# Kernel optimization log

Measured on AMD Instinct MI355X. Metric: run time of the kernel, lower is better.

Reference implementation:

```python
import jax, jax.numpy as jnp
import numpy as np

SEQ_LEN = 8192
D_MODEL = 1024
D_K = 128
D_V = 128


def setup_inputs() -> dict:
    key = jax.random.key(0)
    kx, kq, kk, kv = jax.random.split(key, 4)
    # xavier-uniform scale for (out, in) linear weights
    def xavier(k, out_f, in_f):
        lim = np.sqrt(6.0 / (in_f + out_f))
        return jax.random.uniform(k, (out_f, in_f), jnp.float32, -lim, lim)
    return {
        "X": jax.random.normal(kx, (SEQ_LEN, D_MODEL), jnp.float32),
        "Wq": xavier(kq, D_K, D_MODEL),
        "Wk": xavier(kk, D_K, D_MODEL),
        "Wv": xavier(kv, D_V, D_MODEL),
    }


def reference(X, Wq, Wk, Wv):
    # X: (S, d_model); W*: (d_k, d_model) torch Linear weights (y = x @ W.T)
    S = X.shape[0]
    Q = X @ Wq.T                      # (S, d_k)
    K = X @ Wk.T                      # (S, d_k)
    V = X @ Wv.T                      # (S, d_v)
    scale = jnp.sqrt(jnp.asarray(D_K, X.dtype))
    scores = (Q @ K.T) / scale        # (S, S)
    causal = jnp.tril(jnp.ones((S, S), bool))
    scores = jnp.where(causal, scores, -jnp.inf)
    weights = jax.nn.softmax(scores, axis=1)
    # dropout p=0.0 -> identity
    Z = weights @ V                   # (S, d_v)
    return Z
```

## Files before the change

### kernel.cpp

```cpp
#include <hip/hip_runtime.h>
#include <hip/hip_bf16.h>

#define S_LEN 8192
#define DM    1024
#define DK    128
#define KSTR  136
#define VSTR  72
#define SLOTD 2112
#define NCMAX 16

typedef __attribute__((ext_vector_type(8))) short bf16x8;
typedef __attribute__((ext_vector_type(8))) _Float16 f16x8;
typedef __attribute__((ext_vector_type(4))) float f32x4;
typedef __attribute__((ext_vector_type(16))) float f32x16;

__device__ __forceinline__ f32x4 mfma16f(f16x8 a, f16x8 b, f32x4 c) {
    return __builtin_amdgcn_mfma_f32_16x16x32_f16(a, b, c, 0, 0, 0);
}
__device__ __forceinline__ f32x16 mfma32(bf16x8 a, bf16x8 b, f32x16 c) {
    return __builtin_amdgcn_mfma_f32_32x32x16_bf16(a, b, c, 0, 0, 0);
}

__device__ __forceinline__ ushort f2bf(float f) {
    unsigned u = __builtin_bit_cast(unsigned, f);
    u += 0x7FFFu + ((u >> 16) & 1u);
    return (ushort)(u >> 16);
}

__device__ __forceinline__ ushort f2h(float f) {
    return __builtin_bit_cast(ushort, (_Float16)f);
}

__device__ __forceinline__ uint cvt_pk_bf16(float a, float b) {
    uint r;
    asm("v_cvt_pk_bf16_f32 %0, %1, %2" : "=v"(r) : "v"(a), "v"(b));
    return r;
}

__global__ __launch_bounds__(256, 1)
void convert_w_kernel(const float* __restrict__ Wq,
                      const float* __restrict__ Wk,
                      const float* __restrict__ Wv,
                      _Float16* __restrict__ Wh) {
    const int NW4 = DK * DM / 4;
    const int i = blockIdx.x * 256 + threadIdx.x;
    const int which = i / NW4;
    const int off = i - which * NW4;
    const float4 v = ((const float4*)(which == 0 ? Wq : (which == 1 ? Wk : Wv)))[off];
    union { _Float16 h[4]; uint2 u; } p;
    p.h[0] = (_Float16)v.x; p.h[1] = (_Float16)v.y;
    p.h[2] = (_Float16)v.z; p.h[3] = (_Float16)v.w;
    *(uint2*)(Wh + (size_t)which * (DK * DM) + (size_t)off * 4) = p.u;
}

__global__ __launch_bounds__(256)
void proj_gemm_kernel(const float* __restrict__ X,
                      const _Float16* __restrict__ Wh,
                      ushort* __restrict__ Qb,
                      ushort* __restrict__ Kb,
                      ushort* __restrict__ Vtb) {
    __shared__ _Float16 Ash[2][16 * 32];
    __shared__ _Float16 Bsh[2][384 * 32];

    const int tid  = threadIdx.x;
    const int lane = tid & 63;
    const int quad = lane >> 4;
    const int l15  = lane & 15;
    const int wv   = tid >> 6;
    const int m0   = blockIdx.x * 16;
    const int arow = tid >> 3, ac4 = tid & 7;

    f32x4 acc[3][2];
#pragma unroll
    for (int nb = 0; nb < 3; ++nb)
#pragma unroll
        for (int ni = 0; ni < 2; ++ni) acc[nb][ni] = (f32x4){0.f, 0.f, 0.f, 0.f};

#define STAGE_B(KK, BUF)                                                       \
    {                                                                          \
        _Pragma("unroll")                                                      \
        for (int s_ = tid; s_ < 1536; s_ += 256) {                             \
            const int row_ = s_ >> 2, sg_ = s_ & 3;                            \
            __builtin_amdgcn_global_load_lds(                                  \
                (const __attribute__((address_space(1))) void*)(Wh + (size_t)row_ * DM + (KK) + sg_ * 8), \
                (__attribute__((address_space(3))) void*)(Bsh[BUF] + s_ * 8), 16, 0, 0); \
        }                                                                      \
    }
#define LOAD_A(DST, KK)                                                        \
    if (tid < 128) (DST) = *(const float4*)(X + (size_t)(m0 + arow) * DM + (KK) + ac4 * 4);
#define WRITE_A(SRC, BUF)                                                      \
    if (tid < 128) {                                                           \
        union { _Float16 h[4]; uint2 u; } pa_;                                 \
        pa_.h[0] = (_Float16)(SRC).x; pa_.h[1] = (_Float16)(SRC).y;            \
        pa_.h[2] = (_Float16)(SRC).z; pa_.h[3] = (_Float16)(SRC).w;            \
        *(uint2*)(Ash[BUF] + arow * 32 + ac4 * 4) = pa_.u;                     \
    }
#define COMPUTE(BUF)                                                           \
    {                                                                          \
        const f16x8 af_ = *(const f16x8*)(Ash[BUF] + l15 * 32 + quad * 8);     \
        _Pragma("unroll")                                                      \
        for (int nb_ = 0; nb_ < 3; ++nb_)                                      \
            _Pragma("unroll")                                                  \
            for (int ni_ = 0; ni_ < 2; ++ni_) {                                \
                const f16x8 bf_ = *(const f16x8*)(Bsh[BUF] + (nb_ * 128 + wv * 32 + ni_ * 16 + l15) * 32 + quad * 8); \
                acc[nb_][ni_] = mfma16f(af_, bf_, acc[nb_][ni_]);              \
            }                                                                  \
    }

    float4 ra, rb;
    LOAD_A(ra, 0)
    LOAD_A(rb, 32)
    STAGE_B(0, 0)
    WRITE_A(ra, 0)
    __syncthreads();

    for (int kk = 0; kk < DM; kk += 64) {
        if (kk + 32 < DM) STAGE_B(kk + 32, 1)
        if (kk + 64 < DM) LOAD_A(ra, kk + 64)
        COMPUTE(0)
        if (kk + 32 < DM) WRITE_A(rb, 1)
        __syncthreads();
        if (kk + 32 < DM) {
            if (kk + 64 < DM) STAGE_B(kk + 64, 0)
            if (kk + 96 < DM) LOAD_A(rb, kk + 96)
            COMPUTE(1)
            if (kk + 64 < DM) WRITE_A(ra, 0)
            __syncthreads();
        }
    }
#undef STAGE_B
#undef LOAD_A
#undef WRITE_A
#undef COMPUTE

    const float scq = 0.088388347648318447f * 1.4426950408889634f;
#pragma unroll
    for (int ni = 0; ni < 2; ++ni) {
        const int n = wv * 32 + ni * 16 + l15;
#pragma unroll
        for (int r = 0; r < 4; ++r)
            Qb[(size_t)(m0 + quad * 4 + r) * DK + n] = f2bf(acc[0][ni][r] * scq);
#pragma unroll
        for (int r = 0; r < 4; ++r)
            Kb[(size_t)(m0 + quad * 4 + r) * DK + n] = f2bf(acc[1][ni][r]);
        union { ushort h[4]; uint2 u; } p;
#pragma unroll
        for (int r = 0; r < 4; ++r) p.h[r] = f2bf(acc[2][ni][r]);
        *(uint2*)(Vtb + (size_t)n * S_LEN + m0 + quad * 4) = p.u;
    }
}

__global__ __launch_bounds__(256, 2)
void flash_partial_kernel(const ushort* __restrict__ Qg,
                          const ushort* __restrict__ Kg,
                          const ushort* __restrict__ Vtg,
                          float* __restrict__ Part) {
    __shared__ __align__(16) ushort Ks [2][64 * KSTR];
    __shared__ __align__(16) ushort Vts[2][128 * VSTR];

    int rem = 543 - (int)blockIdx.x;
    int qb = 0;
    for (;;) {
        const int nc = (2 * qb + 9) >> 3;
        if (rem < nc) break;
        rem -= nc; ++qb;
    }
    const int NC    = (2 * qb + 9) >> 3;
    const int chunk = rem;
    const int nkt   = 2 * qb + 2;
    const int kt_lo = chunk * nkt / NC;
    const int kt_hi = (chunk + 1) * nkt / NC;

    const int tid  = threadIdx.x;
    const int wv   = tid >> 6;
    const int lane = tid & 63;
    const int l31  = lane & 31;
    const int hi   = lane >> 5;
    const int q0w  = qb * 128 + wv * 32;
    const int qrow = q0w + l31;

    bf16x8 qf[8];
    {
        const ushort* qp = Qg + (size_t)qrow * DK + hi * 8;
#pragma unroll
        for (int i = 0; i < 8; ++i) qf[i] = *(const bf16x8*)(qp + i * 16);
    }

    float m_ = -__builtin_inff();
    float l_ = 0.f;
    f32x16 acc[4];
#pragma unroll
    for (int dt = 0; dt < 4; ++dt)
#pragma unroll
        for (int j = 0; j < 16; ++j) acc[dt][j] = 0.f;

    bf16x8 stg[8];
#define LOAD_TILE(K0)                                                          \
    {                                                                          \
        const int k0_ = (K0);                                                  \
        _Pragma("unroll")                                                      \
        for (int i = 0; i < 8; ++i) {                                          \
            const int c = tid + (i << 8);                                      \
            if (c < 1024) {                                                    \
                const int row = c >> 4, ch = c & 15;                           \
                stg[i] = *(const bf16x8*)(Kg + (size_t)(k0_ + row) * DK + ch * 8); \
            } else {                                                           \
                const int cc = c - 1024;                                       \
                const int row = cc >> 3, ch = cc & 7;                          \
                stg[i] = *(const bf16x8*)(Vtg + (size_t)row * S_LEN + k0_ + ch * 8); \
            }                                                                  \
        }                                                                      \
    }
#define WRITE_BUF(B)                                                           \
    {                                                                          \
        ushort* Kb_ = Ks[B]; ushort* Vb_ = Vts[B];                             \
        _Pragma("unroll")                                                      \
        for (int i = 0; i < 8; ++i) {                                          \
            const int c = tid + (i << 8);                                      \
            if (c < 1024) {                                                    \
                const int row = c >> 4, ch = c & 15;                           \
                *(bf16x8*)(Kb_ + row * KSTR + ch * 8) = stg[i];                \
            } else {                                                           \
                const int cc = c - 1024;                                       \
                const int row = cc >> 3, ch = cc & 7;                          \
                const int s_lo = ((ch & 1) << 2) + (((ch >> 1) & 1) << 4) + ((ch >> 2) << 5); \
                union { bf16x8 v; uint2 q2[2]; } u;                            \
                u.v = stg[i];                                                  \
                ushort* vb = Vb_ + row * VSTR + s_lo;                          \
                *(uint2*)vb       = u.q2[0];                                   \
                *(uint2*)(vb + 8) = u.q2[1];                                   \
            }                                                                  \
        }                                                                      \
    }

    LOAD_TILE(kt_lo * 64)
    WRITE_BUF(0)
    if (kt_lo + 1 < kt_hi) LOAD_TILE((kt_lo + 1) * 64)
    __syncthreads();

    for (int kt = kt_lo; kt < kt_hi; ++kt) {
        const int k0 = kt * 64;
        const int cb = (kt - kt_lo) & 1;
        const ushort* ks = Ks[cb];
        const ushort* vs = Vts[cb];
        const bool prc = (k0 <= q0w);

        f32x16 Sr0, Sr1;
        if (prc) {
            __builtin_amdgcn_s_setprio(1);
#pragma unroll
            for (int j = 0; j < 16; ++j) { Sr0[j] = 0.f; Sr1[j] = 0.f; }
            const ushort* ka0 = ks + l31 * KSTR + hi * 8;
            const ushort* ka1 = ka0 + 32 * KSTR;
#pragma unroll
            for (int i = 0; i < 8; ++i)
                Sr0 = mfma32(*(const bf16x8*)(ka0 + i * 16), qf[i], Sr0);
#pragma unroll
            for (int i = 0; i < 8; ++i)
                Sr1 = mfma32(*(const bf16x8*)(ka1 + i * 16), qf[i], Sr1);
            __builtin_amdgcn_s_setprio(0);
        }

        if (kt + 1 < kt_hi) {
            WRITE_BUF(cb ^ 1)
            if (kt + 2 < kt_hi) LOAD_TILE((kt + 2) * 64)
        }

        if (prc) {
            if (k0 + 63 > q0w) {
#pragma unroll
                for (int r = 0; r < 16; ++r) {
                    const int krow = (r & 3) + 8 * (r >> 2) + 4 * hi;
                    if (k0 + krow > qrow)      Sr0[r] = -__builtin_inff();
                    if (k0 + 32 + krow > qrow) Sr1[r] = -__builtin_inff();
                }
            }

            float pmax = Sr0[0];
#pragma unroll
            for (int r = 1; r < 16; ++r) pmax = fmaxf(pmax, Sr0[r]);
#pragma unroll
            for (int r = 0; r < 16; ++r) pmax = fmaxf(pmax, Sr1[r]);
            pmax = fmaxf(pmax, __shfl_xor(pmax, 32));
            if (__any(pmax > m_ + 8.f)) {
                const float mnew = fmaxf(m_, pmax);
                const float al = __builtin_amdgcn_exp2f(m_ - mnew);
                m_ = mnew;
                l_ *= al;
#pragma unroll
                for (int dt = 0; dt < 4; ++dt)
#pragma unroll
                    for (int j = 0; j < 16; ++j) acc[dt][j] *= al;
            }
            float rs = 0.f;
            uint pfa[16];
            {
                float p0[16], p1[16];
#pragma unroll
                for (int r = 0; r < 16; ++r) { p0[r] = __builtin_amdgcn_exp2f(Sr0[r] - m_); rs += p0[r]; }
#pragma unroll
                for (int r = 0; r < 16; ++r) { p1[r] = __builtin_amdgcn_exp2f(Sr1[r] - m_); rs += p1[r]; }
#pragma unroll
                for (int j = 0; j < 4; ++j) {
                    pfa[j]      = cvt_pk_bf16(p0[2 * j],     p0[2 * j + 1]);
                    pfa[4 + j]  = cvt_pk_bf16(p0[8 + 2 * j], p0[8 + 2 * j + 1]);
                    pfa[8 + j]  = cvt_pk_bf16(p1[2 * j],     p1[2 * j + 1]);
                    pfa[12 + j] = cvt_pk_bf16(p1[8 + 2 * j], p1[8 + 2 * j + 1]);
                }
            }
            rs += __shfl_xor(rs, 32);
            l_ += rs;

            __builtin_amdgcn_s_setprio(1);
#pragma unroll
            for (int kc = 0; kc < 4; ++kc) {
                union { uint u[4]; bf16x8 v; } pu;
#pragma unroll
                for (int j = 0; j < 4; ++j) pu.u[j] = pfa[4 * kc + j];
                const ushort* va = vs + l31 * VSTR + kc * 16 + hi * 8;
#pragma unroll
                for (int dt = 0; dt < 4; ++dt)
                    acc[dt] = mfma32(*(const bf16x8*)(va + dt * 32 * VSTR), pu.v, acc[dt]);
            }
            __builtin_amdgcn_s_setprio(0);
        }
        __syncthreads();
    }
#undef LOAD_TILE
#undef WRITE_BUF

    const int qt32 = qb * 4 + wv;
    float* slot = Part + (size_t)(qt32 * NCMAX + chunk) * SLOTD;
    if (hi == 0) {
        slot[l31]      = m_;
        slot[32 + l31] = l_;
    }
    uint* slotO = (uint*)(slot + 64);
#pragma unroll
    for (int dt = 0; dt < 4; ++dt)
#pragma unroll
        for (int s = 0; s < 4; ++s) {
            uint2 w;
            w.x = (uint)f2h(acc[dt][4 * s])     | ((uint)f2h(acc[dt][4 * s + 1]) << 16);
            w.y = (uint)f2h(acc[dt][4 * s + 2]) | ((uint)f2h(acc[dt][4 * s + 3]) << 16);
            *(uint2*)(slotO + l31 * 64 + dt * 16 + s * 4 + hi * 2) = w;
        }
}

__global__ __launch_bounds__(256)
void flash_merge_kernel(const float* __restrict__ Part, float* __restrict__ Out) {
    __shared__ float Ms[32], Ls[32];
    __shared__ float Sc[16][32];
    const int qt   = blockIdx.x >> 1;
    const int half = blockIdx.x & 1;
    const int qb = qt >> 2;
    const int P  = (2 * qb + 9) >> 3;
    const int q0 = qt * 32;
    const int tid = threadIdx.x;
    const float* base = Part + (size_t)qt * NCMAX * SLOTD;

    if (tid < 32) {
        float M = -__builtin_inff();
        for (int p = 0; p < P; ++p) M = fmaxf(M, base[p * SLOTD + tid]);
        float L = 0.f;
        for (int p = 0; p < P; ++p)
            L += base[p * SLOTD + 32 + tid] * exp2f(base[p * SLOTD + tid] - M);
        Ms[tid] = M; Ls[tid] = L;
    }
    __syncthreads();
    for (int j = tid; j < 512; j += 256) {
        const int p = j >> 5, row = j & 31;
        Sc[p][row] = (p < P) ? exp2f(base[p * SLOTD + row] - Ms[row]) : 0.f;
    }
    __syncthreads();

#pragma unroll
    for (int j = tid; j < 1024; j += 256) {
        const int row = j >> 5, c2 = (j & 31) + half * 32;
        float o0 = 0.f, o1 = 0.f;
        for (int p = 0; p < P; ++p) {
            const uint u = ((const uint*)(base + p * SLOTD + 64))[row * 64 + c2];
            const float sc = Sc[p][row];
            o0 += (float)__builtin_bit_cast(_Float16, (ushort)(u & 0xFFFF)) * sc;
            o1 += (float)__builtin_bit_cast(_Float16, (ushort)(u >> 16)) * sc;
        }
        const float inv = 1.0f / Ls[row];
        float2 o; o.x = o0 * inv; o.y = o1 * inv;
        *(float2*)(Out + (size_t)(q0 + row) * DK + c2 * 2) = o;
    }
}

extern "C" void kernel_launch(void* const* d_in, const int* in_sizes, int n_in,
                              void* d_out, int out_size, void* d_ws, size_t ws_size,
                              hipStream_t stream) {
    const float* X  = (const float*)d_in[0];
    const float* Wq = (const float*)d_in[1];
    const float* Wk = (const float*)d_in[2];
    const float* Wv = (const float*)d_in[3];
    ushort* ws  = (ushort*)d_ws;
    ushort* Qb  = ws;
    ushort* Kb  = ws + (size_t)S_LEN * DK;
    ushort* Vtb = ws + 2 * (size_t)S_LEN * DK;
    _Float16* Wh = (_Float16*)(ws + 3 * (size_t)S_LEN * DK);
    float* Part = (float*)(Wh + (size_t)3 * DK * DM);
    float* Out = (float*)d_out;

    convert_w_kernel<<<384, 256, 0, stream>>>(Wq, Wk, Wv, Wh);
    proj_gemm_kernel<<<512, 256, 0, stream>>>(X, Wh, Qb, Kb, Vtb);
    flash_partial_kernel<<<544, 256, 0, stream>>>(Qb, Kb, Vtb, Part);
    flash_merge_kernel<<<512, 256, 0, stream>>>(Part, Out);
}
```

Measured before the change: 169.4 us.

## Fuse weight conversion into larger-tile projection GEMM and shrink flash KV tile

Removes the separate weight-conversion kernel. The projection GEMM now loads fp32 weights directly and uses 64x128 tiles with 32x32 f16 MFMAs, one output matrix per block, and a block-index swizzle. In the flash kernel the K/V tile drops from 64 to 32 keys with smaller LDS buffers, and launch bounds rise to 4 blocks per CU for higher occupancy. The trade-offs are more loop iterations and syncs per key range, and X being re-read and re-converted three times in the projection.

```diff
diff --git a/kernel.cpp b/kernel.cpp
--- a/kernel.cpp
+++ b/kernel.cpp
@@ -5,7 +5,8 @@
 #define DM    1024
 #define DK    128
 #define KSTR  136
-#define VSTR  72
+#define VSTR  40
+#define ASTR  68
 #define SLOTD 2112
 #define NCMAX 16
 
@@ -14,11 +15,11 @@
 typedef __attribute__((ext_vector_type(4))) float f32x4;
 typedef __attribute__((ext_vector_type(16))) float f32x16;
 
-__device__ __forceinline__ f32x4 mfma16f(f16x8 a, f16x8 b, f32x4 c) {
-    return __builtin_amdgcn_mfma_f32_16x16x32_f16(a, b, c, 0, 0, 0);
-}
 __device__ __forceinline__ f32x16 mfma32(bf16x8 a, bf16x8 b, f32x16 c) {
     return __builtin_amdgcn_mfma_f32_32x32x16_bf16(a, b, c, 0, 0, 0);
+}
+__device__ __forceinline__ f32x16 mfma32f(f16x8 a, f16x8 b, f32x16 c) {
+    return __builtin_amdgcn_mfma_f32_32x32x16_f16(a, b, c, 0, 0, 0);
 }
 
 __device__ __forceinline__ ushort f2bf(float f) {
@@ -37,125 +38,132 @@
     return r;
 }
 
-__global__ __launch_bounds__(256, 1)
-void convert_w_kernel(const float* __restrict__ Wq,
+__global__ __launch_bounds__(256)
+void proj_gemm_kernel(const float* __restrict__ X,
+                      const float* __restrict__ Wq,
                       const float* __restrict__ Wk,
                       const float* __restrict__ Wv,
-                      _Float16* __restrict__ Wh) {
-    const int NW4 = DK * DM / 4;
-    const int i = blockIdx.x * 256 + threadIdx.x;
-    const int which = i / NW4;
-    const int off = i - which * NW4;
-    const float4 v = ((const float4*)(which == 0 ? Wq : (which == 1 ? Wk : Wv)))[off];
-    union { _Float16 h[4]; uint2 u; } p;
-    p.h[0] = (_Float16)v.x; p.h[1] = (_Float16)v.y;
-    p.h[2] = (_Float16)v.z; p.h[3] = (_Float16)v.w;
-    *(uint2*)(Wh + (size_t)which * (DK * DM) + (size_t)off * 4) = p.u;
-}
-
-__global__ __launch_bounds__(256)
-void proj_gemm_kernel(const float* __restrict__ X,
-                      const _Float16* __restrict__ Wh,
                       ushort* __restrict__ Qb,
                       ushort* __restrict__ Kb,
                       ushort* __restrict__ Vtb) {
-    __shared__ _Float16 Ash[2][16 * 32];
-    __shared__ _Float16 Bsh[2][384 * 32];
+    __shared__ _Float16 Ash[2][64 * ASTR];
+    __shared__ _Float16 Bsh[2][128 * ASTR];
+
+    const int raw = blockIdx.x;
+    const int swz = (raw & 7) * 48 + (raw >> 3);
+    const int mb  = swz / 3;
+    const int which = swz - mb * 3;
+    const float* Wsrc = (which == 0) ? Wq : (which == 1 ? Wk : Wv);
+    const int m0 = mb * 64;
 
     const int tid  = threadIdx.x;
     const int lane = tid & 63;
-    const int quad = lane >> 4;
-    const int l15  = lane & 15;
+    const int l31  = lane & 31;
+    const int hi   = lane >> 5;
     const int wv   = tid >> 6;
-    const int m0   = blockIdx.x * 16;
-    const int arow = tid >> 3, ac4 = tid & 7;
-
-    f32x4 acc[3][2];
-#pragma unroll
-    for (int nb = 0; nb < 3; ++nb)
-#pragma unroll
-        for (int ni = 0; ni < 2; ++ni) acc[nb][ni] = (f32x4){0.f, 0.f, 0.f, 0.f};
-
-#define STAGE_B(KK, BUF)                                                       \
+    const int wm   = wv & 1;
+    const int wn   = wv >> 1;
+
+    f32x16 acc[2];
+#pragma unroll
+    for (int j = 0; j < 2; ++j)
+#pragma unroll
+        for (int r = 0; r < 16; ++r) acc[j][r] = 0.f;
+
+    float4 ra[4], rb[8];
+#define LOADR(KK)                                                              \
     {                                                                          \
         _Pragma("unroll")                                                      \
-        for (int s_ = tid; s_ < 1536; s_ += 256) {                             \
-            const int row_ = s_ >> 2, sg_ = s_ & 3;                            \
-            __builtin_amdgcn_global_load_lds(                                  \
-                (const __attribute__((address_space(1))) void*)(Wh + (size_t)row_ * DM + (KK) + sg_ * 8), \
-                (__attribute__((address_space(3))) void*)(Bsh[BUF] + s_ * 8), 16, 0, 0); \
-        }                                                                      \
-    }
-#define LOAD_A(DST, KK)                                                        \
-    if (tid < 128) (DST) = *(const float4*)(X + (size_t)(m0 + arow) * DM + (KK) + ac4 * 4);
-#define WRITE_A(SRC, BUF)                                                      \
-    if (tid < 128) {                                                           \
-        union { _Float16 h[4]; uint2 u; } pa_;                                 \
-        pa_.h[0] = (_Float16)(SRC).x; pa_.h[1] = (_Float16)(SRC).y;            \
-        pa_.h[2] = (_Float16)(SRC).z; pa_.h[3] = (_Float16)(SRC).w;            \
-        *(uint2*)(Ash[BUF] + arow * 32 + ac4 * 4) = pa_.u;                     \
+        for (int i = 0; i < 4; ++i) {                                          \
+            const int s = tid + (i << 8);                                      \
+            ra[i] = *(const float4*)(X + (size_t)(m0 + (s >> 4)) * DM + (KK) + (s & 15) * 4); \
+        }                                                                      \
+        _Pragma("unroll")                                                      \
+        for (int i = 0; i < 8; ++i) {                                          \
+            const int s = tid + (i << 8);                                      \
+            rb[i] = *(const float4*)(Wsrc + (size_t)(s >> 4) * DM + (KK) + (s & 15) * 4); \
+        }                                                                      \
+    }
+#define WRITEB(BUF)                                                            \
+    {                                                                          \
+        _Pragma("unroll")                                                      \
+        for (int i = 0; i < 4; ++i) {                                          \
+            const int s = tid + (i << 8);                                      \
+            union { _Float16 h[4]; uint2 u; } p_;                              \
+            p_.h[0] = (_Float16)ra[i].x; p_.h[1] = (_Float16)ra[i].y;          \
+            p_.h[2] = (_Float16)ra[i].z; p_.h[3] = (_Float16)ra[i].w;          \
+            *(uint2*)(Ash[BUF] + (s >> 4) * ASTR + (s & 15) * 4) = p_.u;       \
+        }                                                                      \
+        _Pragma("unroll")                                                      \
+        for (int i = 0; i < 8; ++i) {                                          \
+            const int s = tid + (i << 8);                                      \
+            union { _Float16 h[4]; uint2 u; } p_;                              \
+            p_.h[0] = (_Float16)rb[i].x; p_.h[1] = (_Float16)rb[i].y;          \
+            p_.h[2] = (_Float16)rb[i].z; p_.h[3] = (_Float16)rb[i].w;          \
+            *(uint2*)(Bsh[BUF] + (s >> 4) * ASTR + (s & 15) * 4) = p_.u;       \
+        }                                                                      \
     }
 #define COMPUTE(BUF)                                                           \
     {                                                                          \
-        const f16x8 af_ = *(const f16x8*)(Ash[BUF] + l15 * 32 + quad * 8);     \
-        _Pragma("unroll")                                                      \
-        for (int nb_ = 0; nb_ < 3; ++nb_)                                      \
+        const _Float16* As_ = Ash[BUF] + (wm * 32 + l31) * ASTR + hi * 8;      \
+        const _Float16* Bs_ = Bsh[BUF] + (wn * 64 + l31) * ASTR + hi * 8;      \
+        __builtin_amdgcn_s_setprio(1);                                         \
+        _Pragma("unroll")                                                      \
+        for (int ks = 0; ks < 4; ++ks) {                                       \
+            const f16x8 af_ = *(const f16x8*)(As_ + ks * 16);                  \
             _Pragma("unroll")                                                  \
-            for (int ni_ = 0; ni_ < 2; ++ni_) {                                \
-                const f16x8 bf_ = *(const f16x8*)(Bsh[BUF] + (nb_ * 128 + wv * 32 + ni_ * 16 + l15) * 32 + quad * 8); \
-                acc[nb_][ni_] = mfma16f(af_, bf_, acc[nb_][ni_]);              \
+            for (int j = 0; j < 2; ++j) {                                      \
+                const f16x8 bf_ = *(const f16x8*)(Bs_ + j * 32 * ASTR + ks * 16); \
+                acc[j] = mfma32f(af_, bf_, acc[j]);                            \
             }                                                                  \
-    }
-
-    float4 ra, rb;
-    LOAD_A(ra, 0)
-    LOAD_A(rb, 32)
-    STAGE_B(0, 0)
-    WRITE_A(ra, 0)
+        }                                                                      \
+        __builtin_amdgcn_s_setprio(0);                                         \
+    }
+
+    LOADR(0)
+    WRITEB(0)
     __syncthreads();
-
-    for (int kk = 0; kk < DM; kk += 64) {
-        if (kk + 32 < DM) STAGE_B(kk + 32, 1)
-        if (kk + 64 < DM) LOAD_A(ra, kk + 64)
-        COMPUTE(0)
-        if (kk + 32 < DM) WRITE_A(rb, 1)
+    for (int it = 0; it < 16; ++it) {
+        const int cur = it & 1;
+        if (it < 15) LOADR((it + 1) * 64)
+        COMPUTE(cur)
+        if (it < 15) WRITEB(cur ^ 1)
         __syncthreads();
-        if (kk + 32 < DM) {
-            if (kk + 64 < DM) STAGE_B(kk + 64, 0)
-            if (kk + 96 < DM) LOAD_A(rb, kk + 96)
-            COMPUTE(1)
-            if (kk + 64 < DM) WRITE_A(ra, 0)
-            __syncthreads();
-        }
-    }
-#undef STAGE_B
-#undef LOAD_A
-#undef WRITE_A
+    }
+#undef LOADR
+#undef WRITEB
 #undef COMPUTE
 
     const float scq = 0.088388347648318447f * 1.4426950408889634f;
 #pragma unroll
-    for (int ni = 0; ni < 2; ++ni) {
-        const int n = wv * 32 + ni * 16 + l15;
-#pragma unroll
-        for (int r = 0; r < 4; ++r)
-            Qb[(size_t)(m0 + quad * 4 + r) * DK + n] = f2bf(acc[0][ni][r] * scq);
-#pragma unroll
-        for (int r = 0; r < 4; ++r)
-            Kb[(size_t)(m0 + quad * 4 + r) * DK + n] = f2bf(acc[1][ni][r]);
-        union { ushort h[4]; uint2 u; } p;
-#pragma unroll
-        for (int r = 0; r < 4; ++r) p.h[r] = f2bf(acc[2][ni][r]);
-        *(uint2*)(Vtb + (size_t)n * S_LEN + m0 + quad * 4) = p.u;
-    }
-}
-
-__global__ __launch_bounds__(256, 2)
+    for (int j = 0; j < 2; ++j) {
+        const int n = wn * 64 + j * 32 + l31;
+        if (which == 2) {
+#pragma unroll
+            for (int rq = 0; rq < 4; ++rq) {
+                union { ushort h[4]; uint2 u; } p;
+#pragma unroll
+                for (int d = 0; d < 4; ++d) p.h[d] = f2bf(acc[j][4 * rq + d]);
+                *(uint2*)(Vtb + (size_t)n * S_LEN + m0 + wm * 32 + 8 * rq + 4 * hi) = p.u;
+            }
+        } else {
+            ushort* Ob = (which == 0) ? Qb : Kb;
+            const float sc = (which == 0) ? scq : 1.0f;
+#pragma unroll
+            for (int r = 0; r < 16; ++r) {
+                const int row = m0 + wm * 32 + (r & 3) + 8 * (r >> 2) + 4 * hi;
+                Ob[(size_t)row * DK + n] = f2bf(acc[j][r] * sc);
+            }
+        }
+    }
+}
+
+__global__ __launch_bounds__(256, 4)
 void flash_partial_kernel(const ushort* __restrict__ Qg,
                           const ushort* __restrict__ Kg,
                           const ushort* __restrict__ Vtg,
                           float* __restrict__ Part) {
-    __shared__ __align__(16) ushort Ks [2][64 * KSTR];
+    __shared__ __align__(16) ushort Ks [2][32 * KSTR];
     __shared__ __align__(16) ushort Vts[2][128 * VSTR];
 
     int rem = 543 - (int)blockIdx.x;
@@ -167,7 +175,7 @@
     }
     const int NC    = (2 * qb + 9) >> 3;
     const int chunk = rem;
-    const int nkt   = 2 * qb + 2;
+    const int nkt   = 4 * qb + 4;
     const int kt_lo = chunk * nkt / NC;
     const int kt_hi = (chunk + 1) * nkt / NC;
 
@@ -194,19 +202,19 @@
 #pragma unroll
         for (int j = 0; j < 16; ++j) acc[dt][j] = 0.f;
 
-    bf16x8 stg[8];
+    bf16x8 stg[4];
 #define LOAD_TILE(K0)                                                          \
     {                                                                          \
         const int k0_ = (K0);                                                  \
         _Pragma("unroll")                                                      \
-        for (int i = 0; i < 8; ++i) {                                          \
+        for (int i = 0; i < 4; ++i) {                                          \
             const int c = tid + (i << 8);                                      \
-            if (c < 1024) {                                                    \
+            if (c < 512) {                                                     \
                 const int row = c >> 4, ch = c & 15;                           \
                 stg[i] = *(const bf16x8*)(Kg + (size_t)(k0_ + row) * DK + ch * 8); \
             } else {                                                           \
-                const int cc = c - 1024;                                       \
-                const int row = cc >> 3, ch = cc & 7;                          \
+                const int cc = c - 512;                                        \
+                const int row = cc >> 2, ch = cc & 3;                          \
                 stg[i] = *(const bf16x8*)(Vtg + (size_t)row * S_LEN + k0_ + ch * 8); \
             }                                                                  \
         }                                                                      \
@@ -215,15 +223,15 @@
     {                                                                          \
         ushort* Kb_ = Ks[B]; ushort* Vb_ = Vts[B];                             \
         _Pragma("unroll")                                                      \
-        for (int i = 0; i < 8; ++i) {                                          \
+        for (int i = 0; i < 4; ++i) {                                          \
             const int c = tid + (i << 8);                                      \
-            if (c < 1024) {                                                    \
+            if (c < 512) {                                                     \
                 const int row = c >> 4, ch = c & 15;                           \
                 *(bf16x8*)(Kb_ + row * KSTR + ch * 8) = stg[i];                \
             } else {                                                           \
-                const int cc = c - 1024;                                       \
-                const int row = cc >> 3, ch = cc & 7;                          \
-                const int s_lo = ((ch & 1) << 2) + (((ch >> 1) & 1) << 4) + ((ch >> 2) << 5); \
+                const int cc = c - 512;                                        \
+                const int row = cc >> 2, ch = cc & 3;                          \
+                const int s_lo = ((ch & 1) << 2) + ((ch >> 1) << 4);           \
                 union { bf16x8 v; uint2 q2[2]; } u;                            \
                 u.v = stg[i];                                                  \
                 ushort* vb = Vb_ + row * VSTR + s_lo;                          \
@@ -233,54 +241,47 @@
         }                                                                      \
     }
 
-    LOAD_TILE(kt_lo * 64)
+    LOAD_TILE(kt_lo * 32)
     WRITE_BUF(0)
-    if (kt_lo + 1 < kt_hi) LOAD_TILE((kt_lo + 1) * 64)
+    if (kt_lo + 1 < kt_hi) LOAD_TILE((kt_lo + 1) * 32)
     __syncthreads();
 
     for (int kt = kt_lo; kt < kt_hi; ++kt) {
-        const int k0 = kt * 64;
+        const int k0 = kt * 32;
         const int cb = (kt - kt_lo) & 1;
         const ushort* ks = Ks[cb];
         const ushort* vs = Vts[cb];
         const bool prc = (k0 <= q0w);
 
-        f32x16 Sr0, Sr1;
+        f32x16 Sr0;
         if (prc) {
             __builtin_amdgcn_s_setprio(1);
 #pragma unroll
-            for (int j = 0; j < 16; ++j) { Sr0[j] = 0.f; Sr1[j] = 0.f; }
+            for (int j = 0; j < 16; ++j) Sr0[j] = 0.f;
             const ushort* ka0 = ks + l31 * KSTR + hi * 8;
-            const ushort* ka1 = ka0 + 32 * KSTR;
 #pragma unroll
             for (int i = 0; i < 8; ++i)
                 Sr0 = mfma32(*(const bf16x8*)(ka0 + i * 16), qf[i], Sr0);
-#pragma unroll
-            for (int i = 0; i < 8; ++i)
-                Sr1 = mfma32(*(const bf16x8*)(ka1 + i * 16), qf[i], Sr1);
             __builtin_amdgcn_s_setprio(0);
         }
 
         if (kt + 1 < kt_hi) {
             WRITE_BUF(cb ^ 1)
-            if (kt + 2 < kt_hi) LOAD_TILE((kt + 2) * 64)
+            if (kt + 2 < kt_hi) LOAD_TILE((kt + 2) * 32)
         }
 
         if (prc) {
-            if (k0 + 63 > q0w) {
+            if (k0 + 31 > q0w) {
 #pragma unroll
                 for (int r = 0; r < 16; ++r) {
                     const int krow = (r & 3) + 8 * (r >> 2) + 4 * hi;
-                    if (k0 + krow > qrow)      Sr0[r] = -__builtin_inff();
-                    if (k0 + 32 + krow > qrow) Sr1[r] = -__builtin_inff();
+                    if (k0 + krow > qrow) Sr0[r] = -__builtin_inff();
                 }
             }
 
             float pmax = Sr0[0];
 #pragma unroll
             for (int r = 1; r < 16; ++r) pmax = fmaxf(pmax, Sr0[r]);
-#pragma unroll
-            for (int r = 0; r < 16; ++r) pmax = fmaxf(pmax, Sr1[r]);
             pmax = fmaxf(pmax, __shfl_xor(pmax, 32));
             if (__any(pmax > m_ + 8.f)) {
                 const float mnew = fmaxf(m_, pmax);
@@ -293,19 +294,15 @@
                     for (int j = 0; j < 16; ++j) acc[dt][j] *= al;
             }
             float rs = 0.f;
-            uint pfa[16];
+            uint pfa[8];
             {
-                float p0[16], p1[16];
+                float p0[16];
 #pragma unroll
                 for (int r = 0; r < 16; ++r) { p0[r] = __builtin_amdgcn_exp2f(Sr0[r] - m_); rs += p0[r]; }
 #pragma unroll
-                for (int r = 0; r < 16; ++r) { p1[r] = __builtin_amdgcn_exp2f(Sr1[r] - m_); rs += p1[r]; }
-#pragma unroll
                 for (int j = 0; j < 4; ++j) {
-                    pfa[j]      = cvt_pk_bf16(p0[2 * j],     p0[2 * j + 1]);
-                    pfa[4 + j]  = cvt_pk_bf16(p0[8 + 2 * j], p0[8 + 2 * j + 1]);
-                    pfa[8 + j]  = cvt_pk_bf16(p1[2 * j],     p1[2 * j + 1]);
-                    pfa[12 + j] = cvt_pk_bf16(p1[8 + 2 * j], p1[8 + 2 * j + 1]);
+                    pfa[j]     = cvt_pk_bf16(p0[2 * j],     p0[2 * j + 1]);
+                    pfa[4 + j] = cvt_pk_bf16(p0[8 + 2 * j], p0[8 + 2 * j + 1]);
                 }
             }
             rs += __shfl_xor(rs, 32);
@@ -313,7 +310,7 @@
 
             __builtin_amdgcn_s_setprio(1);
 #pragma unroll
-            for (int kc = 0; kc < 4; ++kc) {
+            for (int kc = 0; kc < 2; ++kc) {
                 union { uint u[4]; bf16x8 v; } pu;
 #pragma unroll
                 for (int j = 0; j < 4; ++j) pu.u[j] = pfa[4 * kc + j];
@@ -401,12 +398,10 @@
     ushort* Qb  = ws;
     ushort* Kb  = ws + (size_t)S_LEN * DK;
     ushort* Vtb = ws + 2 * (size_t)S_LEN * DK;
-    _Float16* Wh = (_Float16*)(ws + 3 * (size_t)S_LEN * DK);
-    float* Part = (float*)(Wh + (size_t)3 * DK * DM);
+    float* Part = (float*)(ws + 3 * (size_t)S_LEN * DK);
     float* Out = (float*)d_out;
 
-    convert_w_kernel<<<384, 256, 0, stream>>>(Wq, Wk, Wv, Wh);
-    proj_gemm_kernel<<<512, 256, 0, stream>>>(X, Wh, Qb, Kb, Vtb);
+    proj_gemm_kernel<<<384, 256, 0, stream>>>(X, Wq, Wk, Wv, Qb, Kb, Vtb);
     flash_partial_kernel<<<544, 256, 0, stream>>>(Qb, Kb, Vtb, Part);
     flash_merge_kernel<<<512, 256, 0, stream>>>(Part, Out);
 }
```

Result: slower. 245.4 us (+44.9%).
